# Kernel tuning notes

Hardware: AMD Instinct MI355X
Metric: run time of the kernel (lower is better)

## Reference

```python
import jax, jax.numpy as jnp
import numpy as np

B, T, C, H = 2, 2048, 1024, 16
HD = C // H  # head dim = 64


def setup_inputs() -> dict:
    key = jax.random.key(0)
    ks = jax.random.split(key, 12)
    s = 1.0 / np.sqrt(C)
    return {
        "q": jax.random.normal(ks[0], (B, T, C), jnp.float32),
        "k": jax.random.normal(ks[1], (B, T, C), jnp.float32),
        "v": jax.random.normal(ks[2], (B, T, C), jnp.float32),
        "attn_bias": jax.random.normal(ks[3], (1, H, T, T), jnp.float32),
        "Wq": jax.random.normal(ks[4], (C, C), jnp.float32) * s,
        "bq": jnp.zeros((C,), jnp.float32),
        "Wk": jax.random.normal(ks[5], (C, C), jnp.float32) * s,
        "bk": jnp.zeros((C,), jnp.float32),
        "Wv": jax.random.normal(ks[6], (C, C), jnp.float32) * s,
        "bv": jnp.zeros((C,), jnp.float32),
        "Wp": jax.random.normal(ks[7], (C, C), jnp.float32) * s,
        "bp": jnp.zeros((C,), jnp.float32),
    }


def reference(q, k, v, attn_bias, Wq, bq, Wk, bk, Wv, bv, Wp, bp):
    # Linear projections (torch Linear: x @ W.T + b), then split heads -> [B,H,T,HD]
    def split_heads(x):
        return x.reshape(B, T, H, HD).transpose(0, 2, 1, 3)

    qh = split_heads(q @ Wq.T + bq)
    kh = split_heads(k @ Wk.T + bk)
    vh = split_heads(v @ Wv.T + bv)

    scale = 1.0 / np.sqrt(HD)
    att = jnp.einsum("bhqd,bhkd->bhqk", qh, kh) * scale  # [B,H,T,T]

    causal = jnp.tril(jnp.ones((T, T), dtype=bool))  # mask[:, :, -Tq:, :Tk]
    att_scores = jnp.where(causal[None, None], att, -jnp.inf)
    att_scores = att_scores + attn_bias

    att_probs = jax.nn.softmax(att_scores, axis=-1)
    y = jnp.einsum("bhqk,bhkd->bhqd", att_probs, vh)
    y = y.transpose(0, 2, 1, 3).reshape(B, T, C)
    y = y @ Wp.T + bp  # dropout p=0.0
    return (y, att_scores)
```

## Files before the change

### kernel.cpp

```cpp
#include <hip/hip_runtime.h>
#include <hip/hip_bf16.h>
#include <math.h>

#define B_ 2
#define T_ 2048
#define C_ 1024
#define H_ 16
#define HD_ 64
#define M_ (B_*T_)
#define K_ 1024

#define SCORE_NINF (-3.0e38f)

#define PART_BH 33792

typedef __attribute__((ext_vector_type(8))) short bf16x8;
typedef __attribute__((ext_vector_type(8))) unsigned short u16x8;
typedef __attribute__((ext_vector_type(4))) float f32x4;

__device__ __forceinline__ ushort f2bf_rne(float x) {
    union { float f; unsigned u; } c; c.f = x;
    unsigned r = c.u + 0x7fffu + ((c.u >> 16) & 1u);
    return (ushort)(r >> 16);
}
__device__ __forceinline__ float bfval(ushort h) {
    union { float f; unsigned u; } c; c.u = ((unsigned)h) << 16; return c.f;
}
__device__ __forceinline__ ushort bf16_hi(float x) {
    union { float f; unsigned u; } c; c.f = x; return (ushort)(c.u >> 16);
}
__device__ __forceinline__ void nt_store_f4(float* p, f32x4 v) {
    __builtin_nontemporal_store(v, (f32x4*)p);
}

__device__ __forceinline__ void gload_lds16(const void* g, void* l) {
    __builtin_amdgcn_global_load_lds(
        (const __attribute__((address_space(1))) unsigned int*)g,
        (__attribute__((address_space(3))) unsigned int*)l, 16, 0, 0);
}

__global__ __launch_bounds__(256) void split4_kernel(
    const float* __restrict__ W0, const float* __restrict__ W1,
    const float* __restrict__ W2, const float* __restrict__ W3,
    ushort* __restrict__ h0, ushort* __restrict__ l0,
    ushort* __restrict__ h1, ushort* __restrict__ l1,
    ushort* __restrict__ h2, ushort* __restrict__ l2,
    ushort* __restrict__ h3, ushort* __restrict__ l3)
{
    const int wsel = blockIdx.x >> 10;
    const float* src = (wsel == 0) ? W0 : (wsel == 1) ? W1 : (wsel == 2) ? W2 : W3;
    ushort* hi = (wsel == 0) ? h0 : (wsel == 1) ? h1 : (wsel == 2) ? h2 : h3;
    ushort* lo = (wsel == 0) ? l0 : (wsel == 1) ? l1 : (wsel == 2) ? l2 : l3;
    const int i = (((blockIdx.x & 1023) * 256) + threadIdx.x) * 4;
    const float4 x = *(const float4*)&src[i];
    ushort4 h, l;
    h.x = f2bf_rne(x.x); l.x = f2bf_rne(x.x - bfval(h.x));
    h.y = f2bf_rne(x.y); l.y = f2bf_rne(x.y - bfval(h.y));
    h.z = f2bf_rne(x.z); l.z = f2bf_rne(x.z - bfval(h.z));
    h.w = f2bf_rne(x.w); l.w = f2bf_rne(x.w - bfval(h.w));
    *(ushort4*)&hi[i] = h;
    *(ushort4*)&lo[i] = l;
}

__global__ __launch_bounds__(256) void gemm_qkv(
    const float* __restrict__ Xq, const float* __restrict__ Xk, const float* __restrict__ Xv,
    const ushort* __restrict__ Wqh, const ushort* __restrict__ Wql,
    const ushort* __restrict__ Wkh, const ushort* __restrict__ Wkl,
    const ushort* __restrict__ Wvh, const ushort* __restrict__ Wvl,
    const float* __restrict__ bq, const float* __restrict__ bk, const float* __restrict__ bv,
    ushort* __restrict__ qo_hi, ushort* __restrict__ qo_lo,
    ushort* __restrict__ ko_hi, ushort* __restrict__ ko_lo,
    ushort* __restrict__ vo_hi, ushort* __restrict__ vo_lo)
{
    constexpr int APITCH = 40;
    __shared__ ushort AhS[128 * APITCH];
    __shared__ ushort AlS[128 * APITCH];
    __shared__ ushort BhS[128 * 32];
    __shared__ ushort BlS[128 * 32];

    const int z = blockIdx.z;
    const float*  Xf = (z == 0) ? Xq : (z == 1) ? Xk : Xv;
    const ushort* Wh = (z == 0) ? Wqh : (z == 1) ? Wkh : Wvh;
    const ushort* Wl = (z == 0) ? Wql : (z == 1) ? Wkl : Wvl;
    const float*  bias = (z == 0) ? bq : (z == 1) ? bk : bv;
    ushort* out_hi = (z == 0) ? qo_hi : (z == 1) ? ko_hi : vo_hi;
    ushort* out_lo = (z == 0) ? qo_lo : (z == 1) ? ko_lo : vo_lo;

    const int tid  = threadIdx.x;
    const int lane = tid & 63;
    const int w    = tid >> 6;
    const int lr   = lane & 15, lk = lane >> 4;
    const int wr   = w >> 1,    wc = w & 1;
    const int bm   = blockIdx.x * 128;
    const int bn   = blockIdx.y * 128;

    f32x4 acc[4][4];
    #pragma unroll
    for (int i = 0; i < 4; ++i)
        #pragma unroll
        for (int j = 0; j < 4; ++j) acc[i][j] = (f32x4){0.f, 0.f, 0.f, 0.f};

    const int ar   = tid >> 1;
    const int aseg = (tid & 1) * 16;

    for (int k0 = 0; k0 < K_; k0 += 32) {
        {
            const int r0 = w * 32;
            #pragma unroll
            for (int ii = 0; ii < 2; ++ii) {
                const int rr = r0 + ii * 16;
                const size_t goff = (size_t)(bn + rr + (lane >> 2)) * K_ + k0 + (lane & 3) * 8;
                gload_lds16(Wh + goff, &BhS[rr * 32]);
                gload_lds16(Wl + goff, &BlS[rr * 32]);
            }
        }
        {
            const float* xp = Xf + (size_t)(bm + ar) * K_ + aseg + k0;
            const float4 f0 = *(const float4*)(xp + 0);
            const float4 f1 = *(const float4*)(xp + 4);
            const float4 f2 = *(const float4*)(xp + 8);
            const float4 f3 = *(const float4*)(xp + 12);
            float xs[16];
            xs[0]=f0.x; xs[1]=f0.y; xs[2]=f0.z; xs[3]=f0.w;
            xs[4]=f1.x; xs[5]=f1.y; xs[6]=f1.z; xs[7]=f1.w;
            xs[8]=f2.x; xs[9]=f2.y; xs[10]=f2.z; xs[11]=f2.w;
            xs[12]=f3.x; xs[13]=f3.y; xs[14]=f3.z; xs[15]=f3.w;
            u16x8 hv[2], lv[2];
            #pragma unroll
            for (int e = 0; e < 16; ++e) {
                const ushort hh = f2bf_rne(xs[e]);
                const ushort ll = f2bf_rne(xs[e] - bfval(hh));
                hv[e >> 3][e & 7] = hh;
                lv[e >> 3][e & 7] = ll;
            }
            *(u16x8*)&AhS[ar * APITCH + aseg]     = hv[0];
            *(u16x8*)&AhS[ar * APITCH + aseg + 8] = hv[1];
            *(u16x8*)&AlS[ar * APITCH + aseg]     = lv[0];
            *(u16x8*)&AlS[ar * APITCH + aseg + 8] = lv[1];
        }
        __syncthreads();

        bf16x8 afr[4][2], bfr[4][2];
        #pragma unroll
        for (int i = 0; i < 4; ++i) {
            const int arow = wr * 64 + i * 16 + lr;
            afr[i][0] = *(const bf16x8*)&AhS[arow * APITCH + lk * 8];
            afr[i][1] = *(const bf16x8*)&AlS[arow * APITCH + lk * 8];
        }
        #pragma unroll
        for (int j = 0; j < 4; ++j) {
            const int brow = wc * 64 + j * 16 + lr;
            bfr[j][0] = *(const bf16x8*)&BhS[brow * 32 + lk * 8];
            bfr[j][1] = *(const bf16x8*)&BlS[brow * 32 + lk * 8];
        }
        #pragma unroll
        for (int i = 0; i < 4; ++i)
            #pragma unroll
            for (int j = 0; j < 4; ++j) {
                acc[i][j] = __builtin_amdgcn_mfma_f32_16x16x32_bf16(afr[i][0], bfr[j][0], acc[i][j], 0, 0, 0);
                acc[i][j] = __builtin_amdgcn_mfma_f32_16x16x32_bf16(afr[i][0], bfr[j][1], acc[i][j], 0, 0, 0);
                acc[i][j] = __builtin_amdgcn_mfma_f32_16x16x32_bf16(afr[i][1], bfr[j][0], acc[i][j], 0, 0, 0);
            }
        __syncthreads();
    }

    const int m0 = bm + wr * 64;
    const int n0 = bn + wc * 64;
    #pragma unroll
    for (int j = 0; j < 4; ++j) {
        const int n = n0 + j * 16 + lr;
        const float bias_n = bias[n];
        #pragma unroll
        for (int i = 0; i < 4; ++i) {
            if (z == 2) {
                const int mbase = m0 + i * 16 + lk * 4;
                const int bb = mbase >> 11, t0 = mbase & 2047;
                const int hh = n >> 6, dd = n & 63;
                ushort4 h4, l4;
                float o;
                o = acc[i][j][0] + bias_n; h4.x = f2bf_rne(o); l4.x = f2bf_rne(o - bfval(h4.x));
                o = acc[i][j][1] + bias_n; h4.y = f2bf_rne(o); l4.y = f2bf_rne(o - bfval(h4.y));
                o = acc[i][j][2] + bias_n; h4.z = f2bf_rne(o); l4.z = f2bf_rne(o - bfval(h4.z));
                o = acc[i][j][3] + bias_n; h4.w = f2bf_rne(o); l4.w = f2bf_rne(o - bfval(h4.w));
                const size_t base = (((size_t)(bb * H_ + hh)) * HD_ + dd) * T_ + t0;
                *(ushort4*)&out_hi[base] = h4;
                *(ushort4*)&out_lo[base] = l4;
            } else {
                #pragma unroll
                for (int q = 0; q < 4; ++q) {
                    const int m = m0 + i * 16 + lk * 4 + q;
                    const float o = acc[i][j][q] + bias_n;
                    const int bb = m >> 11, tt = m & 2047;
                    const int hh = n >> 6, dd = n & 63;
                    const size_t idx = (((size_t)(bb * H_ + hh)) * T_ + tt) * HD_ + dd;
                    const ushort hv2 = f2bf_rne(o);
                    out_hi[idx] = hv2;
                    out_lo[idx] = f2bf_rne(o - bfval(hv2));
                }
            }
        }
    }
}

__global__ __launch_bounds__(256) void gemm_final(
    const ushort* __restrict__ Xh, const ushort* __restrict__ Xl,
    const ushort* __restrict__ Wh, const ushort* __restrict__ Wl,
    const float*  __restrict__ bias, float* __restrict__ outf)
{
    __shared__ ushort AhS[128 * 32];
    __shared__ ushort AlS[128 * 32];
    __shared__ ushort BhS[128 * 32];
    __shared__ ushort BlS[128 * 32];

    const int tid  = threadIdx.x;
    const int lane = tid & 63;
    const int w    = tid >> 6;
    const int lr   = lane & 15, lk = lane >> 4;
    const int wr   = w >> 1,    wc = w & 1;
    const int bm   = blockIdx.x * 128;
    const int bn   = blockIdx.y * 128;

    f32x4 acc[4][4];
    #pragma unroll
    for (int i = 0; i < 4; ++i)
        #pragma unroll
        for (int j = 0; j < 4; ++j) acc[i][j] = (f32x4){0.f, 0.f, 0.f, 0.f};

    for (int k0 = 0; k0 < K_; k0 += 32) {
        const int r0 = w * 32;
        #pragma unroll
        for (int ii = 0; ii < 2; ++ii) {
            const int rr = r0 + ii * 16;
            const size_t goffB = (size_t)(bn + rr + (lane >> 2)) * K_ + k0 + (lane & 3) * 8;
            gload_lds16(Wh + goffB, &BhS[rr * 32]);
            gload_lds16(Wl + goffB, &BlS[rr * 32]);
            const size_t goffA = (size_t)(bm + rr + (lane >> 2)) * K_ + k0 + (lane & 3) * 8;
            gload_lds16(Xh + goffA, &AhS[rr * 32]);
            gload_lds16(Xl + goffA, &AlS[rr * 32]);
        }
        __syncthreads();

        bf16x8 afr[4][2], bfr[4][2];
        #pragma unroll
        for (int i = 0; i < 4; ++i) {
            const int arow = wr * 64 + i * 16 + lr;
            afr[i][0] = *(const bf16x8*)&AhS[arow * 32 + lk * 8];
            afr[i][1] = *(const bf16x8*)&AlS[arow * 32 + lk * 8];
        }
        #pragma unroll
        for (int j = 0; j < 4; ++j) {
            const int brow = wc * 64 + j * 16 + lr;
            bfr[j][0] = *(const bf16x8*)&BhS[brow * 32 + lk * 8];
            bfr[j][1] = *(const bf16x8*)&BlS[brow * 32 + lk * 8];
        }
        #pragma unroll
        for (int i = 0; i < 4; ++i)
            #pragma unroll
            for (int j = 0; j < 4; ++j) {
                acc[i][j] = __builtin_amdgcn_mfma_f32_16x16x32_bf16(afr[i][0], bfr[j][0], acc[i][j], 0, 0, 0);
                acc[i][j] = __builtin_amdgcn_mfma_f32_16x16x32_bf16(afr[i][0], bfr[j][1], acc[i][j], 0, 0, 0);
                acc[i][j] = __builtin_amdgcn_mfma_f32_16x16x32_bf16(afr[i][1], bfr[j][0], acc[i][j], 0, 0, 0);
            }
        __syncthreads();
    }

    const int m0 = bm + wr * 64;
    const int n0 = bn + wc * 64;
    #pragma unroll
    for (int j = 0; j < 4; ++j) {
        const int n = n0 + j * 16 + lr;
        const float bias_n = bias[n];
        #pragma unroll
        for (int i = 0; i < 4; ++i)
            #pragma unroll
            for (int q = 0; q < 4; ++q)
                outf[(size_t)(m0 + i * 16 + lk * 4 + q) * C_ + n] = acc[i][j][q] + bias_n;
    }
}

#define SPITCH 1028

__global__ __launch_bounds__(256) void score_kernel(
    const ushort* __restrict__ q_hi, const ushort* __restrict__ q_lo,
    const ushort* __restrict__ k_hi, const ushort* __restrict__ k_lo,
    const float* __restrict__ bias,
    float* __restrict__ scores, float2* __restrict__ partials)
{
    __shared__ float tile[16 * SPITCH];

    const int tid  = threadIdx.x;
    const int w    = tid >> 6, lane = tid & 63;
    const int lr   = lane & 15, lk = lane >> 4;

    const int bid  = blockIdx.x;
    const int pair = (bid >> 4) * 8 + (bid & 7);
    const int b    = (bid >> 3) & 1;
    const int h    = pair / 192;
    const int r    = pair - h * 192;
    const int bh   = b * 16 + h;
    int s, j;
    if (r < 64) { s = r; j = 0; }
    else        { s = 64 + ((r - 64) >> 1); j = (r - 64) & 1; }
    const int qr0 = s * 16;
    const int cbase = j * 1024;
    const int ktmax = s >> 2;
    const int ktbase = j * 16;

    const ushort* qhb = q_hi + (size_t)bh * T_ * HD_;
    const ushort* qlb = q_lo + (size_t)bh * T_ * HD_;
    const ushort* khb = k_hi + (size_t)bh * T_ * HD_;
    const ushort* klb = k_lo + (size_t)bh * T_ * HD_;

    #pragma unroll
    for (int rr = 0; rr < 4; ++rr) {
        const int row = w * 4 + rr;
        const float* gsrc = bias + ((size_t)h * T_ + qr0 + row) * T_ + cbase + lane * 4;
        #pragma unroll
        for (int ch = 0; ch < 4; ++ch)
            gload_lds16(gsrc + ch * 256, &tile[row * SPITCH + ch * 256]);
    }
    __syncthreads();

    const int qrow = qr0 + lr;
    float2* part_bh = partials + (size_t)bh * PART_BH;
    bf16x8 qf[2][2];
    #pragma unroll
    for (int s2 = 0; s2 < 2; ++s2) {
        const size_t qoff = (size_t)qrow * HD_ + s2 * 32 + lk * 8;
        qf[s2][0] = *(const bf16x8*)&qhb[qoff];
        qf[s2][1] = *(const bf16x8*)&qlb[qoff];
    }
    const f32x4 ninf4 = (f32x4){SCORE_NINF, SCORE_NINF, SCORE_NINF, SCORE_NINF};

    #pragma unroll
    for (int i = 0; i < 4; ++i) {
        const int kt  = ktbase + w * 4 + i;
        const int lc0 = (kt - ktbase) * 64;
        if (kt > ktmax) {
            #pragma unroll
            for (int c = 0; c < 4; ++c)
                *(f32x4*)&tile[lr * SPITCH + lc0 + c * 16 + lk * 4] = ninf4;
            continue;
        }
        const int climit = (kt < ktmax) ? 4 : ((s & 3) + 1);
        f32x4 sc[4];
        #pragma unroll
        for (int c = 0; c < 4; ++c) {
            if (c < climit) {
                f32x4 a = (f32x4){0.f, 0.f, 0.f, 0.f};
                #pragma unroll
                for (int s2 = 0; s2 < 2; ++s2) {
                    const size_t koff = (size_t)(kt * 64 + c * 16 + lr) * HD_ + s2 * 32 + lk * 8;
                    const bf16x8 kfh = *(const bf16x8*)&khb[koff];
                    const bf16x8 kfl = *(const bf16x8*)&klb[koff];
                    a = __builtin_amdgcn_mfma_f32_16x16x32_bf16(kfh, qf[s2][0], a, 0, 0, 0);
                    a = __builtin_amdgcn_mfma_f32_16x16x32_bf16(kfl, qf[s2][0], a, 0, 0, 0);
                    a = __builtin_amdgcn_mfma_f32_16x16x32_bf16(kfh, qf[s2][1], a, 0, 0, 0);
                }
                sc[c] = a;
            }
        }
        float tmax = SCORE_NINF;
        #pragma unroll
        for (int c = 0; c < 4; ++c) {
            const int loff = lr * SPITCH + lc0 + c * 16 + lk * 4;
            if (c < climit) {
                const f32x4 b4 = *(const f32x4*)&tile[loff];
                f32x4 o;
                const int kc0 = kt * 64 + c * 16 + lk * 4;
                #pragma unroll
                for (int q4 = 0; q4 < 4; ++q4) {
                    const float sv = (kc0 + q4 <= qrow) ? sc[c][q4] * 0.125f + b4[q4]
                                                        : SCORE_NINF;
                    sc[c][q4] = sv;
                    tmax = fmaxf(tmax, sv);
                    o[q4] = sv;
                }
                *(f32x4*)&tile[loff] = o;
            } else {
                *(f32x4*)&tile[loff] = ninf4;
            }
        }
        tmax = fmaxf(tmax, __shfl_xor(tmax, 16));
        tmax = fmaxf(tmax, __shfl_xor(tmax, 32));
        float tsum = 0.f;
        #pragma unroll
        for (int c = 0; c < 4; ++c) {
            if (c < climit) {
                tsum += __expf(sc[c][0] - tmax);
                tsum += __expf(sc[c][1] - tmax);
                tsum += __expf(sc[c][2] - tmax);
                tsum += __expf(sc[c][3] - tmax);
            }
        }
        tsum += __shfl_xor(tsum, 16);
        tsum += __shfl_xor(tsum, 32);
        if (lk == 0)
            part_bh[kt * (2080 - 32 * kt) + (qrow - kt * 64)] = make_float2(tmax, tsum);
    }
    __syncthreads();

    #pragma unroll
    for (int row = 0; row < 16; ++row) {
        const f32x4 v = *(const f32x4*)&tile[row * SPITCH + tid * 4];
        *(f32x4*)&scores[((size_t)bh * T_ + qr0 + row) * T_ + cbase + tid * 4] = v;
    }
    if (s < 64) {
        const f32x4 ninf4b = (f32x4){SCORE_NINF, SCORE_NINF, SCORE_NINF, SCORE_NINF};
        #pragma unroll
        for (int row = 0; row < 16; ++row)
            nt_store_f4(&scores[((size_t)bh * T_ + qr0 + row) * T_ + 1024 + tid * 4], ninf4b);
    }
}

__global__ __launch_bounds__(256) void reduce_kernel(
    const float2* __restrict__ partials, float2* __restrict__ ml)
{
    const int gid = blockIdx.x * 256 + threadIdx.x;
    const int bh = gid >> 11, r = gid & 2047;
    const float2* pb = partials + (size_t)bh * PART_BH;
    const int nt = (r >> 6) + 1;
    float M = SCORE_NINF;
    for (int t = 0; t < nt; ++t)
        M = fmaxf(M, pb[t * (2080 - 32 * t) + (r - (t << 6))].x);
    float L = 0.f;
    for (int t = 0; t < nt; ++t) {
        const float2 p = pb[t * (2080 - 32 * t) + (r - (t << 6))];
        L += p.y * __expf(p.x - M);
    }
    ml[gid] = make_float2(M, 1.f / L);
}

#define PVPITCH 260

__global__ __launch_bounds__(256) void pv_kernel(
    const ushort* __restrict__ vt_hi, const ushort* __restrict__ vt_lo,
    const float* __restrict__ scores, const float2* __restrict__ ml,
    ushort* __restrict__ y_hi, ushort* __restrict__ y_lo)
{
    __shared__ float stile[16 * PVPITCH];

    const int tid = threadIdx.x;
    const int w = tid >> 6, lane = tid & 63;
    const int lr = lane & 15, lk = lane >> 4;
    const int bh = 31 - ((int)blockIdx.x >> 6);
    const int p  = (int)blockIdx.x & 63;
    const int h = bh & 15, b = bh >> 4;

    const ushort* vhb = vt_hi + (size_t)bh * HD_ * T_;
    const ushort* vlb = vt_lo + (size_t)bh * HD_ * T_;

    #pragma unroll 1
    for (int half = 0; half < 2; ++half) {
        const int s = half ? (127 - p) : p;
        const int qr0 = s * 16;
        const int ktmax = s >> 2;
        const int nch = (ktmax + 4) >> 2;
        const float2 ml2 = ml[(size_t)bh * 2048 + qr0 + lr];
        const float M = ml2.x, invL = ml2.y;

        f32x4 yacc[4];
        #pragma unroll
        for (int c = 0; c < 4; ++c) yacc[c] = (f32x4){0.f, 0.f, 0.f, 0.f};

        #pragma unroll 1
        for (int ch = 0; ch < nch; ++ch) {
            const int cb = ch * 256;
            #pragma unroll
            for (int rr = 0; rr < 4; ++rr) {
                const int row = w * 4 + rr;
                const float* gsrc = scores + ((size_t)bh * T_ + qr0 + row) * T_ + cb + lane * 4;
                gload_lds16(gsrc, &stile[row * PVPITCH]);
            }
            __syncthreads();

            const int kt = ch * 4 + w;
            if (kt <= ktmax) {
                const int climit = (kt < ktmax) ? 4 : ((s & 3) + 1);
                const int s2max = (climit > 2) ? 2 : 1;
                bf16x8 pa[2][2];
                #pragma unroll
                for (int s2 = 0; s2 < 2; ++s2) {
                    if (s2 < s2max) {
                        const float* lsrc = &stile[lr * PVPITCH + w * 64 + s2 * 32 + lk * 8];
                        const f32x4 l0 = *(const f32x4*)(lsrc);
                        const f32x4 l1 = *(const f32x4*)(lsrc + 4);
                        float xs[8];
                        xs[0]=l0[0]; xs[1]=l0[1]; xs[2]=l0[2]; xs[3]=l0[3];
                        xs[4]=l1[0]; xs[5]=l1[1]; xs[6]=l1[2]; xs[7]=l1[3];
                        bf16x8 ph, pl;
                        #pragma unroll
                        for (int jj = 0; jj < 8; ++jj) {
                            const float pv = __expf(xs[jj] - M);
                            const ushort hv = bf16_hi(pv);
                            ph[jj] = (short)hv;
                            pl[jj] = (short)bf16_hi(pv - bfval(hv));
                        }
                        pa[s2][0] = ph;
                        pa[s2][1] = pl;
                    }
                }
                #pragma unroll
                for (int c2 = 0; c2 < 4; ++c2) {
                    #pragma unroll
                    for (int s2 = 0; s2 < 2; ++s2) {
                        if (s2 < s2max) {
                            const size_t voff = (size_t)(c2 * 16 + lr) * T_ + kt * 64 + s2 * 32 + lk * 8;
                            const bf16x8 vfh = *(const bf16x8*)&vhb[voff];
                            const bf16x8 vfl = *(const bf16x8*)&vlb[voff];
                            yacc[c2] = __builtin_amdgcn_mfma_f32_16x16x32_bf16(pa[s2][0], vfh, yacc[c2], 0, 0, 0);
                            yacc[c2] = __builtin_amdgcn_mfma_f32_16x16x32_bf16(pa[s2][0], vfl, yacc[c2], 0, 0, 0);
                            yacc[c2] = __builtin_amdgcn_mfma_f32_16x16x32_bf16(pa[s2][1], vfh, yacc[c2], 0, 0, 0);
                        }
                    }
                }
            }
            __syncthreads();
        }

        float* mbuf = stile;
        if (w > 0) {
            #pragma unroll
            for (int c2 = 0; c2 < 4; ++c2)
                *(f32x4*)&mbuf[((c2 * 3 + (w - 1)) * 64 + lane) * 4] = yacc[c2];
        }
        __syncthreads();
        if (w == 0) {
            float inv[4];
            #pragma unroll
            for (int q4 = 0; q4 < 4; ++q4) inv[q4] = __shfl(invL, lk * 4 + q4);
            #pragma unroll
            for (int c2 = 0; c2 < 4; ++c2) {
                f32x4 tot = yacc[c2];
                #pragma unroll
                for (int ww = 0; ww < 3; ++ww)
                    tot += *(const f32x4*)&mbuf[((c2 * 3 + ww) * 64 + lane) * 4];
                #pragma unroll
                for (int q4 = 0; q4 < 4; ++q4) {
                    const int yr = qr0 + lk * 4 + q4;
                    const float val = tot[q4] * inv[q4];
                    const size_t yi = ((size_t)b * T_ + yr) * C_ + h * HD_ + c2 * 16 + lr;
                    const ushort hv = f2bf_rne(val);
                    y_hi[yi] = hv;
                    y_lo[yi] = f2bf_rne(val - bfval(hv));
                }
            }
        }
        __syncthreads();
    }
}

extern "C" void kernel_launch(void* const* d_in, const int* in_sizes, int n_in,
                              void* d_out, int out_size, void* d_ws, size_t ws_size,
                              hipStream_t stream) {
    const float* q         = (const float*)d_in[0];
    const float* k         = (const float*)d_in[1];
    const float* v         = (const float*)d_in[2];
    const float* attn_bias = (const float*)d_in[3];
    const float* Wq        = (const float*)d_in[4];
    const float* bq        = (const float*)d_in[5];
    const float* Wk        = (const float*)d_in[6];
    const float* bk        = (const float*)d_in[7];
    const float* Wv        = (const float*)d_in[8];
    const float* bv        = (const float*)d_in[9];
    const float* Wp        = (const float*)d_in[10];
    const float* bp        = (const float*)d_in[11];

    float* y_out      = (float*)d_out;
    float* scores_out = y_out + (size_t)B_*T_*C_;

    ushort* ws = (ushort*)d_ws;
    const size_t NE = (size_t)B_*H_*T_*HD_;
    const size_t WN = (size_t)C_*K_;
    ushort* q_hi  = ws + 0*NE;
    ushort* q_lo  = ws + 1*NE;
    ushort* k_hi  = ws + 2*NE;
    ushort* k_lo  = ws + 3*NE;
    ushort* vt_hi = ws + 4*NE;
    ushort* vt_lo = ws + 5*NE;
    ushort* Wph   = ws + 6*NE;
    ushort* Wpl   = Wph + WN;
    ushort* Wqh   = Wpl + WN;
    ushort* Wql   = Wqh + WN;
    ushort* Wkh   = Wql + WN;
    ushort* Wkl   = Wkh + WN;
    ushort* Wvh   = Wkl + WN;
    ushort* Wvl   = Wvh + WN;
    float2* partials = (float2*)(ws + 6*NE + 2*WN);
    float2* ml    = (float2*)(ws + 0*NE);
    ushort* y_hi  = ws + 1*NE;
    ushort* y_lo  = ws + 2*NE;

    split4_kernel<<<4096, 256, 0, stream>>>(Wq, Wk, Wv, Wp,
        Wqh, Wql, Wkh, Wkl, Wvh, Wvl, Wph, Wpl);

    gemm_qkv<<<dim3(M_/128, C_/128, 3), 256, 0, stream>>>(
        q, k, v, Wqh, Wql, Wkh, Wkl, Wvh, Wvl, bq, bk, bv,
        q_hi, q_lo, k_hi, k_lo, vt_hi, vt_lo);

    score_kernel<<<6144, 256, 0, stream>>>(q_hi, q_lo, k_hi, k_lo, attn_bias,
                                           scores_out, partials);
    reduce_kernel<<<256, 256, 0, stream>>>(partials, ml);
    pv_kernel<<<2048, 256, 0, stream>>>(vt_hi, vt_lo, scores_out, ml, y_hi, y_lo);

    gemm_final<<<dim3(M_/128, C_/128), 256, 0, stream>>>(
        y_hi, y_lo, Wph, Wpl, bp, y_out);
}
```

Before: 619.4 us.

## Pre-split activations to bf16 hi/lo and double-buffer score tiles in PV

The split kernel now also converts the q/k/v activations into bf16 hi/lo pairs, storing them in the scores output buffer as scratch. The QKV GEMM can then load A tiles directly into LDS with global_load_lds instead of converting in registers. Separately, the PV kernel double-buffers the score tile so the next chunk's load overlaps compute, which also drops one barrier per iteration. The trade-off is an extra global write and read of the split activations, plus more LDS use in PV.

```diff
diff --git a/kernel.cpp b/kernel.cpp
--- a/kernel.cpp
+++ b/kernel.cpp
@@ -39,19 +39,35 @@
         (__attribute__((address_space(3))) unsigned int*)l, 16, 0, 0);
 }
 
-__global__ __launch_bounds__(256) void split4_kernel(
-    const float* __restrict__ W0, const float* __restrict__ W1,
-    const float* __restrict__ W2, const float* __restrict__ W3,
-    ushort* __restrict__ h0, ushort* __restrict__ l0,
-    ushort* __restrict__ h1, ushort* __restrict__ l1,
-    ushort* __restrict__ h2, ushort* __restrict__ l2,
-    ushort* __restrict__ h3, ushort* __restrict__ l3)
+__global__ __launch_bounds__(256) void split_many_kernel(
+    const float* __restrict__ S0, const float* __restrict__ S1,
+    const float* __restrict__ S2, const float* __restrict__ S3,
+    const float* __restrict__ S4, const float* __restrict__ S5,
+    const float* __restrict__ S6,
+    ushort* __restrict__ H0, ushort* __restrict__ L0,
+    ushort* __restrict__ H1, ushort* __restrict__ L1,
+    ushort* __restrict__ H2, ushort* __restrict__ L2,
+    ushort* __restrict__ H3, ushort* __restrict__ L3,
+    ushort* __restrict__ H4, ushort* __restrict__ L4,
+    ushort* __restrict__ H5, ushort* __restrict__ L5,
+    ushort* __restrict__ H6, ushort* __restrict__ L6)
 {
-    const int wsel = blockIdx.x >> 10;
-    const float* src = (wsel == 0) ? W0 : (wsel == 1) ? W1 : (wsel == 2) ? W2 : W3;
-    ushort* hi = (wsel == 0) ? h0 : (wsel == 1) ? h1 : (wsel == 2) ? h2 : h3;
-    ushort* lo = (wsel == 0) ? l0 : (wsel == 1) ? l1 : (wsel == 2) ? l2 : l3;
-    const int i = (((blockIdx.x & 1023) * 256) + threadIdx.x) * 4;
+    const int sel = blockIdx.x >> 12;
+    const float* src;
+    ushort *hi, *lo;
+    switch (sel) {
+        case 0: src = S0; hi = H0; lo = L0; break;
+        case 1: src = S1; hi = H1; lo = L1; break;
+        case 2: src = S2; hi = H2; lo = L2; break;
+        case 3: src = S3; hi = H3; lo = L3; break;
+        case 4: src = S4; hi = H4; lo = L4; break;
+        case 5: src = S5; hi = H5; lo = L5; break;
+        default: src = S6; hi = H6; lo = L6; break;
+    }
+    const int nblk = blockIdx.x & 4095;
+    const int nelem = (sel < 4) ? (1 << 20) : (1 << 22);
+    const int i = (nblk * 256 + threadIdx.x) * 4;
+    if (i >= nelem) return;
     const float4 x = *(const float4*)&src[i];
     ushort4 h, l;
     h.x = f2bf_rne(x.x); l.x = f2bf_rne(x.x - bfval(h.x));
@@ -63,7 +79,9 @@
 }
 
 __global__ __launch_bounds__(256) void gemm_qkv(
-    const float* __restrict__ Xq, const float* __restrict__ Xk, const float* __restrict__ Xv,
+    const ushort* __restrict__ Xqh, const ushort* __restrict__ Xql,
+    const ushort* __restrict__ Xkh, const ushort* __restrict__ Xkl,
+    const ushort* __restrict__ Xvh, const ushort* __restrict__ Xvl,
     const ushort* __restrict__ Wqh, const ushort* __restrict__ Wql,
     const ushort* __restrict__ Wkh, const ushort* __restrict__ Wkl,
     const ushort* __restrict__ Wvh, const ushort* __restrict__ Wvl,
@@ -72,14 +90,14 @@
     ushort* __restrict__ ko_hi, ushort* __restrict__ ko_lo,
     ushort* __restrict__ vo_hi, ushort* __restrict__ vo_lo)
 {
-    constexpr int APITCH = 40;
-    __shared__ ushort AhS[128 * APITCH];
-    __shared__ ushort AlS[128 * APITCH];
+    __shared__ ushort AhS[128 * 32];
+    __shared__ ushort AlS[128 * 32];
     __shared__ ushort BhS[128 * 32];
     __shared__ ushort BlS[128 * 32];
 
     const int z = blockIdx.z;
-    const float*  Xf = (z == 0) ? Xq : (z == 1) ? Xk : Xv;
+    const ushort* Xh = (z == 0) ? Xqh : (z == 1) ? Xkh : Xvh;
+    const ushort* Xl = (z == 0) ? Xql : (z == 1) ? Xkl : Xvl;
     const ushort* Wh = (z == 0) ? Wqh : (z == 1) ? Wkh : Wvh;
     const ushort* Wl = (z == 0) ? Wql : (z == 1) ? Wkl : Wvl;
     const float*  bias = (z == 0) ? bq : (z == 1) ? bk : bv;
@@ -100,43 +118,17 @@
         #pragma unroll
         for (int j = 0; j < 4; ++j) acc[i][j] = (f32x4){0.f, 0.f, 0.f, 0.f};
 
-    const int ar   = tid >> 1;
-    const int aseg = (tid & 1) * 16;
-
     for (int k0 = 0; k0 < K_; k0 += 32) {
-        {
-            const int r0 = w * 32;
-            #pragma unroll
-            for (int ii = 0; ii < 2; ++ii) {
-                const int rr = r0 + ii * 16;
-                const size_t goff = (size_t)(bn + rr + (lane >> 2)) * K_ + k0 + (lane & 3) * 8;
-                gload_lds16(Wh + goff, &BhS[rr * 32]);
-                gload_lds16(Wl + goff, &BlS[rr * 32]);
-            }
-        }
-        {
-            const float* xp = Xf + (size_t)(bm + ar) * K_ + aseg + k0;
-            const float4 f0 = *(const float4*)(xp + 0);
-            const float4 f1 = *(const float4*)(xp + 4);
-            const float4 f2 = *(const float4*)(xp + 8);
-            const float4 f3 = *(const float4*)(xp + 12);
-            float xs[16];
-            xs[0]=f0.x; xs[1]=f0.y; xs[2]=f0.z; xs[3]=f0.w;
-            xs[4]=f1.x; xs[5]=f1.y; xs[6]=f1.z; xs[7]=f1.w;
-            xs[8]=f2.x; xs[9]=f2.y; xs[10]=f2.z; xs[11]=f2.w;
-            xs[12]=f3.x; xs[13]=f3.y; xs[14]=f3.z; xs[15]=f3.w;
-            u16x8 hv[2], lv[2];
-            #pragma unroll
-            for (int e = 0; e < 16; ++e) {
-                const ushort hh = f2bf_rne(xs[e]);
-                const ushort ll = f2bf_rne(xs[e] - bfval(hh));
-                hv[e >> 3][e & 7] = hh;
-                lv[e >> 3][e & 7] = ll;
-            }
-            *(u16x8*)&AhS[ar * APITCH + aseg]     = hv[0];
-            *(u16x8*)&AhS[ar * APITCH + aseg + 8] = hv[1];
-            *(u16x8*)&AlS[ar * APITCH + aseg]     = lv[0];
-            *(u16x8*)&AlS[ar * APITCH + aseg + 8] = lv[1];
+        const int r0 = w * 32;
+        #pragma unroll
+        for (int ii = 0; ii < 2; ++ii) {
+            const int rr = r0 + ii * 16;
+            const size_t goffB = (size_t)(bn + rr + (lane >> 2)) * K_ + k0 + (lane & 3) * 8;
+            gload_lds16(Wh + goffB, &BhS[rr * 32]);
+            gload_lds16(Wl + goffB, &BlS[rr * 32]);
+            const size_t goffA = (size_t)(bm + rr + (lane >> 2)) * K_ + k0 + (lane & 3) * 8;
+            gload_lds16(Xh + goffA, &AhS[rr * 32]);
+            gload_lds16(Xl + goffA, &AlS[rr * 32]);
         }
         __syncthreads();
 
@@ -144,8 +136,8 @@
         #pragma unroll
         for (int i = 0; i < 4; ++i) {
             const int arow = wr * 64 + i * 16 + lr;
-            afr[i][0] = *(const bf16x8*)&AhS[arow * APITCH + lk * 8];
-            afr[i][1] = *(const bf16x8*)&AlS[arow * APITCH + lk * 8];
+            afr[i][0] = *(const bf16x8*)&AhS[arow * 32 + lk * 8];
+            afr[i][1] = *(const bf16x8*)&AlS[arow * 32 + lk * 8];
         }
         #pragma unroll
         for (int j = 0; j < 4; ++j) {
@@ -438,7 +430,7 @@
     const float* __restrict__ scores, const float2* __restrict__ ml,
     ushort* __restrict__ y_hi, ushort* __restrict__ y_lo)
 {
-    __shared__ float stile[16 * PVPITCH];
+    __shared__ float stile[2][16 * PVPITCH];
 
     const int tid = threadIdx.x;
     const int w = tid >> 6, lane = tid & 63;
@@ -463,16 +455,28 @@
         #pragma unroll
         for (int c = 0; c < 4; ++c) yacc[c] = (f32x4){0.f, 0.f, 0.f, 0.f};
 
+        {
+            #pragma unroll
+            for (int rr = 0; rr < 4; ++rr) {
+                const int row = w * 4 + rr;
+                const float* gsrc = scores + ((size_t)bh * T_ + qr0 + row) * T_ + lane * 4;
+                gload_lds16(gsrc, &stile[0][row * PVPITCH]);
+            }
+        }
+
+        int cur = 0;
         #pragma unroll 1
         for (int ch = 0; ch < nch; ++ch) {
-            const int cb = ch * 256;
-            #pragma unroll
-            for (int rr = 0; rr < 4; ++rr) {
-                const int row = w * 4 + rr;
-                const float* gsrc = scores + ((size_t)bh * T_ + qr0 + row) * T_ + cb + lane * 4;
-                gload_lds16(gsrc, &stile[row * PVPITCH]);
-            }
             __syncthreads();
+            if (ch + 1 < nch) {
+                const int cb = (ch + 1) * 256;
+                #pragma unroll
+                for (int rr = 0; rr < 4; ++rr) {
+                    const int row = w * 4 + rr;
+                    const float* gsrc = scores + ((size_t)bh * T_ + qr0 + row) * T_ + cb + lane * 4;
+                    gload_lds16(gsrc, &stile[cur ^ 1][row * PVPITCH]);
+                }
+            }
 
             const int kt = ch * 4 + w;
             if (kt <= ktmax) {
@@ -482,7 +486,7 @@
                 #pragma unroll
                 for (int s2 = 0; s2 < 2; ++s2) {
                     if (s2 < s2max) {
-                        const float* lsrc = &stile[lr * PVPITCH + w * 64 + s2 * 32 + lk * 8];
+                        const float* lsrc = &stile[cur][lr * PVPITCH + w * 64 + s2 * 32 + lk * 8];
                         const f32x4 l0 = *(const f32x4*)(lsrc);
                         const f32x4 l1 = *(const f32x4*)(lsrc + 4);
                         float xs[8];
@@ -515,10 +519,11 @@
                     }
                 }
             }
-            __syncthreads();
-        }
-
-        float* mbuf = stile;
+            cur ^= 1;
+        }
+        __syncthreads();
+
+        float* mbuf = &stile[0][0];
         if (w > 0) {
             #pragma unroll
             for (int c2 = 0; c2 < 4; ++c2)
@@ -591,11 +596,22 @@
     ushort* y_hi  = ws + 1*NE;
     ushort* y_lo  = ws + 2*NE;
 
-    split4_kernel<<<4096, 256, 0, stream>>>(Wq, Wk, Wv, Wp,
-        Wqh, Wql, Wkh, Wkl, Wvh, Wvl, Wph, Wpl);
+    ushort* xs    = (ushort*)scores_out;
+    ushort* Xqh   = xs + 0*NE;
+    ushort* Xql   = xs + 1*NE;
+    ushort* Xkh   = xs + 2*NE;
+    ushort* Xkl   = xs + 3*NE;
+    ushort* Xvh   = xs + 4*NE;
+    ushort* Xvl   = xs + 5*NE;
+
+    split_many_kernel<<<7*4096, 256, 0, stream>>>(
+        Wq, Wk, Wv, Wp, q, k, v,
+        Wqh, Wql, Wkh, Wkl, Wvh, Wvl, Wph, Wpl,
+        Xqh, Xql, Xkh, Xkl, Xvh, Xvl);
 
     gemm_qkv<<<dim3(M_/128, C_/128, 3), 256, 0, stream>>>(
-        q, k, v, Wqh, Wql, Wkh, Wkl, Wvh, Wvl, bq, bk, bv,
+        Xqh, Xql, Xkh, Xkl, Xvh, Xvl,
+        Wqh, Wql, Wkh, Wkl, Wvh, Wvl, bq, bk, bv,
         q_hi, q_lo, k_hi, k_lo, vt_hi, vt_lo);
 
     score_kernel<<<6144, 256, 0, stream>>>(q_hi, q_lo, k_hi, k_lo, attn_bias,
```

Result: faster. 594.4 us (-4.0%).
